# Optimization experiments

Measured on AMD Instinct MI355X. Metric: run time of the kernel, lower is better.

Reference implementation:

```python
import jax, jax.numpy as jnp
import numpy as np

L = 2048  # sequence length
V = 2048  # num_tokens == channel width (one-hot embedding)
B = 4     # batch


def _pos_bias(v_table):
    # pos[i,j] = max(i-j, 0); embed via [L,1] table -> [L,L]
    i = jnp.arange(L)
    pos = jnp.maximum(i[:, None] - i[None, :], 0)
    return v_table[pos, 0]


def setup_inputs() -> dict:
    key = jax.random.key(0)
    ks = jax.random.split(key, 11)
    idx = jax.random.randint(ks[0], (B, L), 0, V)
    lin = lambda k, std: (jax.random.normal(k, (V, V), dtype=jnp.float32) * std)
    return {
        "idx": idx,
        # layer_zero: all std=1 (explicit re-init in torch code)
        "Wq0": lin(ks[1], 1.0), "Wk0": lin(ks[2], 1.0), "Wv0": lin(ks[3], 1.0),
        # layer_one: Wk std=1 (re-init), Wv std=0.02 (default init); Wq is zero-fn
        "Wk1": lin(ks[4], 1.0), "Wv1": lin(ks[5], 0.02),
        # layer_two: Wq,Wv std=1 (re-init), Wk std=0.02 (default)
        "Wq2": lin(ks[6], 1.0), "Wk2": lin(ks[7], 0.02), "Wv2": lin(ks[8], 1.0),
        # relative-position embedding tables [L,1], std=0.02
        "v0": jax.random.normal(ks[9], (L, 1), dtype=jnp.float32) * 0.02,
        "v1": jax.random.normal(ks[10], (L, 1), dtype=jnp.float32) * 0.02,
    }


def reference(idx, Wq0, Wk0, Wv0, Wk1, Wv1, Wq2, Wk2, Wv2, v0, v1):
    e = jax.nn.one_hot(idx, V, dtype=jnp.float32)            # [B,L,V]
    tril = jnp.tril(jnp.ones((L, L), dtype=bool))
    p0 = _pos_bias(v0)                                       # [L,L]
    p1 = _pos_bias(v1)

    # layer_zero(e, e): scores = Q@K^T + sum_e(K)[:,None]*pos, tril, @V (no softmax)
    K0 = e @ Wk0.T
    Q0 = e @ Wq0.T
    V0 = e @ Wv0.T
    s0 = jnp.einsum('bqv,bkv->bqk', Q0, K0) + K0.sum(-1)[:, :, None] * p0[None]
    l0 = jnp.where(tril, s0, 0.0) @ V0                       # [B,L,V]

    # layer_one(l0, e): Wq is zero-fn -> only the pos-bias term survives
    K1 = e @ Wk1.T
    V1 = l0 @ Wv1.T
    s1 = K1.sum(-1)[:, :, None] * p1[None]
    l1 = jnp.where(tril, s1, 0.0) @ V1

    # layer_two(e, l1): v is zero-fn -> no pos bias
    K2 = l1 @ Wk2.T
    Q2 = e @ Wq2.T
    V2 = e @ Wv2.T
    s2 = jnp.einsum('bqv,bkv->bqk', Q2, K2)
    logits = jnp.where(tril, s2, 0.0) @ V2                   # [B,L,V]
    return logits
```

## Files before the change

kernel.cpp:

```cpp
#include <hip/hip_runtime.h>

typedef float f32x4 __attribute__((ext_vector_type(4)));
typedef short s16x8 __attribute__((ext_vector_type(8)));

constexpr int L = 2048;
constexpr int V = 2048;
constexpr int NB = 4;
constexpr size_t VV  = (size_t)V * V;
constexpr size_t BLV = (size_t)NB * L * V;
constexpr size_t LV  = (size_t)L * V;

__device__ __forceinline__ unsigned short f2bf(float f) {
    unsigned u = __float_as_uint(f);
    u = (u + 0x7FFFu + ((u >> 16) & 1u)) >> 16;
    return (unsigned short)u;
}
__device__ __forceinline__ float bf2f(unsigned short s) {
    return __uint_as_float(((unsigned)s) << 16);
}

__device__ __forceinline__ void gload16(const unsigned short* g, unsigned short* l) {
    auto gp = (const __attribute__((address_space(1))) unsigned int*)g;
    auto lp = (__attribute__((address_space(3))) unsigned int*)l;
    __builtin_amdgcn_global_load_lds(gp, lp, 16, 0, 0);
}

#define SBAR __builtin_amdgcn_sched_barrier(0)


__device__ __forceinline__ void stage_half(const unsigned short* G, int r0, int k0,
                                           unsigned short* slice, int wave, int lane) {
    int rl = lane >> 2, slot = lane & 3;
    #pragma unroll
    for (int r = 0; r < 2; ++r) {
        int rowl = r * 128 + wave * 16 + rl;
        int colg = k0 + ((slot ^ ((rowl >> 1) & 3)) * 8);
        gload16(G + (size_t)(r0 + rowl) * 2048 + colg,
                slice + (size_t)(r * 128 + wave * 16) * 32);
    }
}

__device__ __forceinline__ s16x8 fragx(const unsigned short* slice, int row, int kc) {
    return *(const s16x8*)&slice[row * 32 + ((kc ^ ((row >> 1) & 3)) * 8)];
}

__device__ __forceinline__ void kloop32(const unsigned short* Ab, const unsigned short* Bb,
                                        int m0, int n0, int NT, unsigned short* lds,
                                        int wave, int lane, int wr, int wc,
                                        f32x4 (&acc)[8][4]) {
    const int r15 = lane & 15, kc = lane >> 4;

    stage_half(Ab, m0, 0,  lds + 0,     wave, lane);
    stage_half(Bb, n0, 0,  lds + 8192,  wave, lane);
    stage_half(Ab, m0, 32, lds + 16384, wave, lane);
    stage_half(Bb, n0, 32, lds + 24576, wave, lane);
    asm volatile("s_waitcnt vmcnt(4)" ::: "memory");
    __builtin_amdgcn_s_barrier();
    SBAR;

    int cb = 0;
    for (int t = 0; t < NT; ++t) {
        const unsigned short* cur = lds + cb * 16384;
        int sb = cb + 2; if (sb >= 3) sb -= 3;
        unsigned short* stg = lds + sb * 16384;
        const bool pre = (t + 2 < NT);
        const int k2 = (t + 2) * 32;

        s16x8 b0[4], a[4], a2[4];
        #pragma unroll
        for (int nf = 0; nf < 4; ++nf)
            b0[nf] = fragx(cur + 8192, wc * 64 + nf * 16 + r15, kc);
        #pragma unroll
        for (int mf = 0; mf < 4; ++mf)
            a[mf] = fragx(cur, wr * 128 + mf * 16 + r15, kc);
        if (pre) stage_half(Ab, m0, k2, stg, wave, lane);
        __builtin_amdgcn_s_setprio(1);
        #pragma unroll
        for (int mf = 0; mf < 4; ++mf)
            #pragma unroll
            for (int nf = 0; nf < 4; ++nf)
                acc[mf][nf] = __builtin_amdgcn_mfma_f32_16x16x32_bf16(a[mf], b0[nf], acc[mf][nf], 0, 0, 0);
        __builtin_amdgcn_s_setprio(0);

        #pragma unroll
        for (int mf = 0; mf < 4; ++mf)
            a2[mf] = fragx(cur, wr * 128 + (mf + 4) * 16 + r15, kc);
        if (pre) stage_half(Bb, n0, k2, stg + 8192, wave, lane);
        __builtin_amdgcn_s_setprio(1);
        #pragma unroll
        for (int mf = 0; mf < 4; ++mf)
            #pragma unroll
            for (int nf = 0; nf < 4; ++nf)
                acc[mf + 4][nf] = __builtin_amdgcn_mfma_f32_16x16x32_bf16(a2[mf], b0[nf], acc[mf + 4][nf], 0, 0, 0);
        __builtin_amdgcn_s_setprio(0);

        if (pre)               { asm volatile("s_waitcnt vmcnt(4)" ::: "memory"); }
        else if (t + 2 == NT)  { asm volatile("s_waitcnt vmcnt(0)" ::: "memory"); }
        __builtin_amdgcn_s_barrier();
        SBAR;
        if (++cb == 3) cb = 0;
    }
}

template<int OUTM, bool TOEP>
__global__ __launch_bounds__(512, 2) void gemm_big(
    const unsigned short* __restrict__ A, size_t sA,
    const unsigned short* __restrict__ B, size_t sB,
    float* __restrict__ outF, unsigned short* __restrict__ outH, size_t sO,
    const int* __restrict__ idxp, const float* __restrict__ ks)
{
    __shared__ __align__(16) unsigned short lds[3 * 16384];

    const int tid  = threadIdx.x;
    const int lane = tid & 63, wave = tid >> 6;
    const int wr = wave >> 2, wc = wave & 3;
    const int bz = blockIdx.z;
    int bx = blockIdx.x, by = blockIdx.y;
    if constexpr (TOEP) { int tswap = bx; bx = by; by = tswap; }
    const int m0 = by * 256, n0 = bx * 256;
    const int r15 = lane & 15, kc = lane >> 4;

    const unsigned short* Ab = A + (size_t)bz * sA;
    const unsigned short* Bb = B + (size_t)bz * sB;
    const int NT = TOEP ? 8 * (bx + 1) : 64;

    f32x4 acc[8][4];
    const f32x4 zf = {0.f, 0.f, 0.f, 0.f};
    #pragma unroll
    for (int i = 0; i < 8; ++i)
        #pragma unroll
        for (int j = 0; j < 4; ++j) acc[i][j] = zf;

    kloop32(Ab, Bb, m0, n0, NT, lds, wave, lane, wr, wc, acc);

    float csc[4];
    if constexpr (TOEP) {
        #pragma unroll
        for (int nf = 0; nf < 4; ++nf) {
            int gcol = n0 + wc * 64 + nf * 16 + r15;
            csc[nf] = ks[idxp[bz * L + gcol]];
        }
    }
    #pragma unroll
    for (int mf = 0; mf < 8; ++mf) {
        #pragma unroll
        for (int r = 0; r < 4; ++r) {
            int grow = m0 + wr * 128 + mf * 16 + kc * 4 + r;
            #pragma unroll
            for (int nf = 0; nf < 4; ++nf) {
                float v = acc[mf][nf][r];
                if constexpr (TOEP) v *= csc[nf];
                int gcol = n0 + wc * 64 + nf * 16 + r15;
                size_t o = (size_t)bz * sO + (size_t)grow * 2048 + gcol;
                if constexpr (OUTM == 0) outF[o] = v;
                else                     outH[o] = f2bf(v);
            }
        }
    }
}

struct PDesc { const unsigned short* A; const unsigned short* B; float* oF; unsigned short* oH; };

__global__ __launch_bounds__(512, 2) void gemm_pre_big(PDesc d0, PDesc d1, PDesc d2) {
    PDesc d = (blockIdx.z == 0) ? d0 : (blockIdx.z == 1) ? d1 : d2;
    __shared__ __align__(16) unsigned short lds[3 * 16384];

    const int tid  = threadIdx.x;
    const int lane = tid & 63, wave = tid >> 6;
    const int wr = wave >> 2, wc = wave & 3;
    const int m0 = blockIdx.y * 256, n0 = blockIdx.x * 256;
    const int r15 = lane & 15, kc = lane >> 4;

    f32x4 acc[8][4];
    const f32x4 zf = {0.f, 0.f, 0.f, 0.f};
    #pragma unroll
    for (int i = 0; i < 8; ++i)
        #pragma unroll
        for (int j = 0; j < 4; ++j) acc[i][j] = zf;

    kloop32(d.A, d.B, m0, n0, 64, lds, wave, lane, wr, wc, acc);

    const bool isF = (d.oF != nullptr);
    #pragma unroll
    for (int mf = 0; mf < 8; ++mf) {
        #pragma unroll
        for (int r = 0; r < 4; ++r) {
            int grow = m0 + wr * 128 + mf * 16 + kc * 4 + r;
            #pragma unroll
            for (int nf = 0; nf < 4; ++nf) {
                float v = acc[mf][nf][r];
                int gcol = n0 + wc * 64 + nf * 16 + r15;
                size_t o = (size_t)grow * 2048 + gcol;
                if (isF) d.oF[o] = v;
                else     d.oH[o] = f2bf(v);
            }
        }
    }
}

__global__ __launch_bounds__(512, 2) void gemm_preK(const unsigned short* __restrict__ A,
                                                    const unsigned short* __restrict__ B,
                                                    float* __restrict__ outP) {
    __shared__ __align__(16) unsigned short lds[3 * 16384];

    const int tid  = threadIdx.x;
    const int lane = tid & 63, wave = tid >> 6;
    const int wr = wave >> 2, wc = wave & 3;
    const int m0 = blockIdx.y * 256, n0 = blockIdx.x * 256;
    const int r15 = lane & 15, kc = lane >> 4;
    const int z = blockIdx.z;

    const unsigned short* Ab = A + z * 512;
    const unsigned short* Bb = B + z * 512;
    float* outF = outP + (size_t)z * VV;

    f32x4 acc[8][4];
    const f32x4 zf = {0.f, 0.f, 0.f, 0.f};
    #pragma unroll
    for (int i = 0; i < 8; ++i)
        #pragma unroll
        for (int j = 0; j < 4; ++j) acc[i][j] = zf;

    kloop32(Ab, Bb, m0, n0, 16, lds, wave, lane, wr, wc, acc);

    #pragma unroll
    for (int mf = 0; mf < 8; ++mf) {
        #pragma unroll
        for (int r = 0; r < 4; ++r) {
            int grow = m0 + wr * 128 + mf * 16 + kc * 4 + r;
            #pragma unroll
            for (int nf = 0; nf < 4; ++nf) {
                int gcol = n0 + wc * 64 + nf * 16 + r15;
                outF[(size_t)grow * 2048 + gcol] = acc[mf][nf][r];
            }
        }
    }
}

__global__ __launch_bounds__(256) void reduce4_cast(const float* __restrict__ P,
                                                    unsigned short* __restrict__ H) {
    int i = blockIdx.x * 256 + threadIdx.x;
    const float4* p0 = (const float4*)P;
    const float4* p1 = (const float4*)(P + VV);
    const float4* p2 = (const float4*)(P + 2 * VV);
    const float4* p3 = (const float4*)(P + 3 * VV);
    float4 a = p0[i], b = p1[i], c = p2[i], d = p3[i];
    ushort4 h;
    h.x = f2bf(a.x + b.x + c.x + d.x);
    h.y = f2bf(a.y + b.y + c.y + d.y);
    h.z = f2bf(a.z + b.z + c.z + d.z);
    h.w = f2bf(a.w + b.w + c.w + d.w);
    ((ushort4*)H)[i] = h;
}


__global__ __launch_bounds__(256) void colsum_atomic(const float* __restrict__ W,
                                                     float* __restrict__ out) {
    int r0 = blockIdx.x * 8;
    int c = threadIdx.x;
    float s[8];
    #pragma unroll
    for (int i = 0; i < 8; ++i) s[i] = 0.f;
    for (int r = 0; r < 8; ++r) {
        const float* row = W + (size_t)(r0 + r) * V;
        #pragma unroll
        for (int i = 0; i < 8; ++i) s[i] += row[c + i * 256];
    }
    #pragma unroll
    for (int i = 0; i < 8; ++i) atomicAdd(&out[c + i * 256], s[i]);
}

__global__ void init_kernel(float* __restrict__ ks0, float* __restrict__ ks1) {
    int i = blockIdx.x * 256 + threadIdx.x;
    if (i < 2048) { ks0[i] = 0.f; ks1[i] = 0.f; }
}

__global__ __launch_bounds__(256) void tb_fill(const float* __restrict__ v1,
                                               unsigned short* __restrict__ TBh) {
    int n = blockIdx.x;
    int c0 = threadIdx.x * 8;
    s16x8 hv;
    #pragma unroll
    for (int i = 0; i < 8; ++i) {
        int k = c0 + i;
        float f = (k <= n) ? v1[n - k] : 0.f;
        hv[i] = (short)f2bf(f);
    }
    *(s16x8*)&TBh[(size_t)n * 2048 + c0] = hv;
}

struct TDesc { const float* A; unsigned short* Th; };

__global__ void transpose_cast_multi(TDesc d0, TDesc d1, TDesc d2, TDesc d3, TDesc d4) {
    TDesc d;
    switch (blockIdx.z) {
        case 0: d = d0; break;
        case 1: d = d1; break;
        case 2: d = d2; break;
        case 3: d = d3; break;
        default: d = d4; break;
    }
    __shared__ float tile[32][33];
    int x = blockIdx.x * 32 + threadIdx.x;
    int y0 = blockIdx.y * 32;
    for (int r = threadIdx.y; r < 32; r += 8)
        tile[r][threadIdx.x] = d.A[(size_t)(y0 + r) * V + x];
    __syncthreads();
    int xo = blockIdx.y * 32 + threadIdx.x;
    int yo0 = blockIdx.x * 32;
    for (int r = threadIdx.y; r < 32; r += 8)
        d.Th[(size_t)(yo0 + r) * V + xo] = f2bf(tile[threadIdx.x][r]);
}

__global__ __launch_bounds__(256) void cast_kernel(const float* __restrict__ A,
                                                   unsigned short* __restrict__ H,
                                                   int n4) {
    int i = blockIdx.x * 256 + threadIdx.x;
    if (i >= n4) return;
    float4 f = ((const float4*)A)[i];
    ushort4 h;
    h.x = f2bf(f.x); h.y = f2bf(f.y); h.z = f2bf(f.z); h.w = f2bf(f.w);
    ((ushort4*)H)[i] = h;
}


__global__ __launch_bounds__(256) void scatterA_kernel(const int* __restrict__ idx,
                                                       const float* __restrict__ G0,
                                                       const float* __restrict__ ks0,
                                                       const float* __restrict__ v0,
                                                       unsigned short* __restrict__ Th) {
    __shared__ float buck[4 * 2048];
    int tid = threadIdx.x;
    const float4 z4 = make_float4(0.f, 0.f, 0.f, 0.f);
    #pragma unroll
    for (int i = 0; i < 8; ++i) ((float4*)buck)[tid + i * 256] = z4;
    __syncthreads();

    int b = blockIdx.y, q0 = blockIdx.x * 4;
    int qr = tid >> 6, lane = tid & 63;
    int q = q0 + qr;
    const int* idxb = idx + b * L;
    int iq = idxb[q];
    float kq = ks0[iq];
    const float* Grow = G0 + (size_t)iq * V;
    float* brow = buck + qr * 2048;

    int k = lane;
    for (; k + 192 <= q; k += 256) {
        int i0 = idxb[k], i1 = idxb[k + 64], i2 = idxb[k + 128], i3 = idxb[k + 192];
        float g0 = Grow[i0], g1 = Grow[i1], g2 = Grow[i2], g3 = Grow[i3];
        float w0 = v0[q - k], w1 = v0[q - k - 64], w2 = v0[q - k - 128], w3 = v0[q - k - 192];
        atomicAdd(&brow[i0], g0 + kq * w0);
        atomicAdd(&brow[i1], g1 + kq * w1);
        atomicAdd(&brow[i2], g2 + kq * w2);
        atomicAdd(&brow[i3], g3 + kq * w3);
    }
    for (; k <= q; k += 64) {
        int ik = idxb[k];
        atomicAdd(&brow[ik], Grow[ik] + kq * v0[q - k]);
    }
    __syncthreads();
    size_t base = ((size_t)b * L + q0) * V;
    #pragma unroll
    for (int it = 0; it < 4; ++it) {
        int i = tid + it * 256;
        s16x8 hv;
        #pragma unroll
        for (int j = 0; j < 8; ++j) hv[j] = (short)f2bf(buck[i * 8 + j]);
        *(s16x8*)&Th[base + (size_t)i * 8] = hv;
    }
}

__global__ __launch_bounds__(256) void scatterC_kernel(const int* __restrict__ idx,
                                                       const unsigned short* __restrict__ T2h,
                                                       unsigned short* __restrict__ Th) {
    __shared__ float buck[4 * 2048];
    int tid = threadIdx.x;
    const float4 z4 = make_float4(0.f, 0.f, 0.f, 0.f);
    #pragma unroll
    for (int i = 0; i < 8; ++i) ((float4*)buck)[tid + i * 256] = z4;
    __syncthreads();

    int b = blockIdx.y, q0 = blockIdx.x * 4;
    int qr = tid >> 6, lane = tid & 63;
    int q = q0 + qr;
    const int* idxb = idx + b * L;
    int iq = idxb[q];
    const unsigned short* Trow = T2h + ((size_t)b * V + iq) * L;
    float* brow = buck + qr * 2048;

    int k = lane;
    for (; k + 192 <= q; k += 256) {
        int i0 = idxb[k], i1 = idxb[k + 64], i2 = idxb[k + 128], i3 = idxb[k + 192];
        float t0 = bf2f(Trow[k]), t1 = bf2f(Trow[k + 64]);
        float t2 = bf2f(Trow[k + 128]), t3 = bf2f(Trow[k + 192]);
        atomicAdd(&brow[i0], t0);
        atomicAdd(&brow[i1], t1);
        atomicAdd(&brow[i2], t2);
        atomicAdd(&brow[i3], t3);
    }
    for (; k <= q; k += 64)
        atomicAdd(&brow[idxb[k]], bf2f(Trow[k]));
    __syncthreads();
    size_t base = ((size_t)b * L + q0) * V;
    #pragma unroll
    for (int it = 0; it < 4; ++it) {
        int i = tid + it * 256;
        s16x8 hv;
        #pragma unroll
        for (int j = 0; j < 8; ++j) hv[j] = (short)f2bf(buck[i * 8 + j]);
        *(s16x8*)&Th[base + (size_t)i * 8] = hv;
    }
}


extern "C" void kernel_launch(void* const* d_in, const int* in_sizes, int n_in,
                              void* d_out, int out_size, void* d_ws, size_t ws_size,
                              hipStream_t stream) {
    (void)in_sizes; (void)n_in; (void)out_size; (void)ws_size;
    const int*   idx = (const int*)d_in[0];
    const float* Wq0 = (const float*)d_in[1];
    const float* Wk0 = (const float*)d_in[2];
    const float* Wv0 = (const float*)d_in[3];
    const float* Wk1 = (const float*)d_in[4];
    const float* Wv1 = (const float*)d_in[5];
    const float* Wq2 = (const float*)d_in[6];
    const float* Wk2 = (const float*)d_in[7];
    const float* Wv2 = (const float*)d_in[8];
    const float* v0  = (const float*)d_in[9];
    const float* v1  = (const float*)d_in[10];
    float* out = (float*)d_out;

    char* W = (char*)d_ws;
    const size_t MiB = 1024 * 1024;

    unsigned short* PPT = (unsigned short*)W;
    unsigned short* TAh = (unsigned short*)W;
    unsigned short* T2h = (unsigned short*)W;
    float* Rp = (float*)(W + 8 * MiB);
    unsigned short* Y1 = (unsigned short*)(W + 64 * MiB);
    unsigned short* Y2 = (unsigned short*)(W + 72 * MiB);
    unsigned short* Uh  = (unsigned short*)(W + 64 * MiB);
    unsigned short* TCh = Uh;
    float* Gf = (float*)(W + 96 * MiB);
    unsigned short* Y4 = (unsigned short*)(W + 112 * MiB);
    unsigned short* X1 = (unsigned short*)(W + 128 * MiB);
    unsigned short* X2 = (unsigned short*)(W + 136 * MiB);
    unsigned short* X3 = (unsigned short*)(W + 144 * MiB);
    unsigned short* X4 = (unsigned short*)(W + 152 * MiB);
    unsigned short* TBh = X3;
    float* ks0 = (float*)(W + 192 * MiB);
    float* ks1 = (float*)(W + 192 * MiB + 16 * 1024);

    dim3 blk(256);

    {
        TDesc t0{Wq0, X1}, t1{Wk0, X2}, t2{Wq2, X3}, t3{Wk2, X4}, t4{Wv0, Y1};
        transpose_cast_multi<<<dim3(64, 64, 5), dim3(32, 8), 0, stream>>>(t0, t1, t2, t3, t4);
    }
    cast_kernel<<<dim3((int)(VV / 4 / 256)), blk, 0, stream>>>(Wv1, Y2, (int)(VV / 4));
    init_kernel<<<dim3(8), blk, 0, stream>>>(ks0, ks1);
    colsum_atomic<<<dim3(256), blk, 0, stream>>>(Wk0, ks0);
    colsum_atomic<<<dim3(256), blk, 0, stream>>>(Wk1, ks1);

    {
        PDesc dG{X1, X2, Gf, nullptr};
        PDesc dM{X3, X4, nullptr, Y4};
        PDesc dP{Y1, Y2, nullptr, PPT};
        gemm_pre_big<<<dim3(8, 8, 3), dim3(512), 0, stream>>>(dG, dM, dP);
    }
    tb_fill<<<dim3(2048), blk, 0, stream>>>(v1, TBh);
    gemm_preK<<<dim3(8, 8, 4), dim3(512), 0, stream>>>(Y4, PPT, Rp);
    reduce4_cast<<<dim3((int)(VV / 4 / 256)), blk, 0, stream>>>(Rp, X1);

    scatterA_kernel<<<dim3(L / 4, NB), blk, 0, stream>>>(idx, Gf, ks0, v0, TAh);

    gemm_big<1, false><<<dim3(8, 8, NB), dim3(512), 0, stream>>>(
        X1, 0, TAh, LV, nullptr, Uh, LV, nullptr, nullptr);

    gemm_big<1, true><<<dim3(8, 8, NB), dim3(512), 0, stream>>>(
        Uh, LV, TBh, 0, nullptr, T2h, LV, idx, ks1);

    scatterC_kernel<<<dim3(L / 4, NB), blk, 0, stream>>>(idx, T2h, TCh);

    cast_kernel<<<dim3((int)(VV / 4 / 256)), blk, 0, stream>>>(Wv2, X2, (int)(VV / 4));

    gemm_big<0, false><<<dim3(8, 32, 1), dim3(512), 0, stream>>>(
        TCh, 0, X2, 0, out, nullptr, 0, nullptr, nullptr);
}
```

Measured before the change: 473.2 us.

## Split triangular Toeplitz GEMM along K, add XCD block swizzle, merge small kernels

The triangular (TOEP) GEMM now splits its K range into two halves across extra grid z-blocks. Each half writes a separate bf16 partial buffer, and scatterC sums the two partials, which evens out load imbalance from the triangular work. Non-Toeplitz GEMMs and the pre-GEMMs remap block indices with an XCD-aware swizzle to improve L2 locality per chiplet. The two cast launches and the two colsum launches are each fused into one, and the Wv2 cast is moved earlier into its own buffer. The cost is an extra partial buffer of writes and reads, plus a second bf16 rounding before the partials are summed.

```diff
diff --git a/kernel.cpp b/kernel.cpp
--- a/kernel.cpp
+++ b/kernel.cpp
@@ -45,15 +45,15 @@
 }
 
 __device__ __forceinline__ void kloop32(const unsigned short* Ab, const unsigned short* Bb,
-                                        int m0, int n0, int NT, unsigned short* lds,
+                                        int m0, int n0, int kt0, int NT, unsigned short* lds,
                                         int wave, int lane, int wr, int wc,
                                         f32x4 (&acc)[8][4]) {
     const int r15 = lane & 15, kc = lane >> 4;
 
-    stage_half(Ab, m0, 0,  lds + 0,     wave, lane);
-    stage_half(Bb, n0, 0,  lds + 8192,  wave, lane);
-    stage_half(Ab, m0, 32, lds + 16384, wave, lane);
-    stage_half(Bb, n0, 32, lds + 24576, wave, lane);
+    stage_half(Ab, m0, kt0 * 32,        lds + 0,     wave, lane);
+    stage_half(Bb, n0, kt0 * 32,        lds + 8192,  wave, lane);
+    stage_half(Ab, m0, (kt0 + 1) * 32,  lds + 16384, wave, lane);
+    stage_half(Bb, n0, (kt0 + 1) * 32,  lds + 24576, wave, lane);
     asm volatile("s_waitcnt vmcnt(4)" ::: "memory");
     __builtin_amdgcn_s_barrier();
     SBAR;
@@ -64,7 +64,7 @@
         int sb = cb + 2; if (sb >= 3) sb -= 3;
         unsigned short* stg = lds + sb * 16384;
         const bool pre = (t + 2 < NT);
-        const int k2 = (t + 2) * 32;
+        const int k2 = (kt0 + t + 2) * 32;
 
         s16x8 b0[4], a[4], a2[4];
         #pragma unroll
@@ -100,6 +100,10 @@
         SBAR;
         if (++cb == 3) cb = 0;
     }
+}
+
+__device__ __forceinline__ int xcd_swz(int flat, int total) {
+    return (flat & 7) * (total >> 3) + (flat >> 3);
 }
 
 template<int OUTM, bool TOEP>
@@ -114,15 +118,33 @@
     const int tid  = threadIdx.x;
     const int lane = tid & 63, wave = tid >> 6;
     const int wr = wave >> 2, wc = wave & 3;
-    const int bz = blockIdx.z;
-    int bx = blockIdx.x, by = blockIdx.y;
-    if constexpr (TOEP) { int tswap = bx; bx = by; by = tswap; }
+    const int r15 = lane & 15, kc = lane >> 4;
+
+    int bx, by, bz, half = 0;
+    if constexpr (TOEP) {
+        bx = blockIdx.y; by = blockIdx.x;
+        bz = blockIdx.z & 3;
+        half = blockIdx.z >> 2;
+    } else {
+        int gx = gridDim.x, gy = gridDim.y;
+        int flat = blockIdx.x + gx * (blockIdx.y + gy * blockIdx.z);
+        int total = gx * gy * gridDim.z;
+        int n2 = xcd_swz(flat, total);
+        bx = n2 % gx; n2 /= gx; by = n2 % gy; bz = n2 / gy;
+    }
     const int m0 = by * 256, n0 = bx * 256;
-    const int r15 = lane & 15, kc = lane >> 4;
+
+    int kt0 = 0, NT;
+    if constexpr (TOEP) {
+        int NTh = 4 * (bx + 1);
+        kt0 = half * NTh;
+        NT = NTh;
+    } else {
+        NT = 64;
+    }
 
     const unsigned short* Ab = A + (size_t)bz * sA;
     const unsigned short* Bb = B + (size_t)bz * sB;
-    const int NT = TOEP ? 8 * (bx + 1) : 64;
 
     f32x4 acc[8][4];
     const f32x4 zf = {0.f, 0.f, 0.f, 0.f};
@@ -131,7 +153,7 @@
         #pragma unroll
         for (int j = 0; j < 4; ++j) acc[i][j] = zf;
 
-    kloop32(Ab, Bb, m0, n0, NT, lds, wave, lane, wr, wc, acc);
+    kloop32(Ab, Bb, m0, n0, kt0, NT, lds, wave, lane, wr, wc, acc);
 
     float csc[4];
     if constexpr (TOEP) {
@@ -141,6 +163,8 @@
             csc[nf] = ks[idxp[bz * L + gcol]];
         }
     }
+    unsigned short* oH = outH;
+    if constexpr (TOEP) oH += (size_t)half * BLV;
     #pragma unroll
     for (int mf = 0; mf < 8; ++mf) {
         #pragma unroll
@@ -153,7 +177,7 @@
                 int gcol = n0 + wc * 64 + nf * 16 + r15;
                 size_t o = (size_t)bz * sO + (size_t)grow * 2048 + gcol;
                 if constexpr (OUTM == 0) outF[o] = v;
-                else                     outH[o] = f2bf(v);
+                else                     oH[o] = f2bf(v);
             }
         }
     }
@@ -162,14 +186,20 @@
 struct PDesc { const unsigned short* A; const unsigned short* B; float* oF; unsigned short* oH; };
 
 __global__ __launch_bounds__(512, 2) void gemm_pre_big(PDesc d0, PDesc d1, PDesc d2) {
-    PDesc d = (blockIdx.z == 0) ? d0 : (blockIdx.z == 1) ? d1 : d2;
     __shared__ __align__(16) unsigned short lds[3 * 16384];
 
     const int tid  = threadIdx.x;
     const int lane = tid & 63, wave = tid >> 6;
     const int wr = wave >> 2, wc = wave & 3;
-    const int m0 = blockIdx.y * 256, n0 = blockIdx.x * 256;
     const int r15 = lane & 15, kc = lane >> 4;
+
+    int flat = blockIdx.x + 8 * (blockIdx.y + 8 * blockIdx.z);
+    int total = 64 * gridDim.z;
+    int n2 = xcd_swz(flat, total);
+    int bx = n2 & 7; n2 >>= 3;
+    int by = n2 & 7; n2 >>= 3;
+    PDesc d = (n2 == 0) ? d0 : (n2 == 1) ? d1 : d2;
+    const int m0 = by * 256, n0 = bx * 256;
 
     f32x4 acc[8][4];
     const f32x4 zf = {0.f, 0.f, 0.f, 0.f};
@@ -178,7 +208,7 @@
         #pragma unroll
         for (int j = 0; j < 4; ++j) acc[i][j] = zf;
 
-    kloop32(d.A, d.B, m0, n0, 64, lds, wave, lane, wr, wc, acc);
+    kloop32(d.A, d.B, m0, n0, 0, 64, lds, wave, lane, wr, wc, acc);
 
     const bool isF = (d.oF != nullptr);
     #pragma unroll
@@ -206,9 +236,14 @@
     const int tid  = threadIdx.x;
     const int lane = tid & 63, wave = tid >> 6;
     const int wr = wave >> 2, wc = wave & 3;
-    const int m0 = blockIdx.y * 256, n0 = blockIdx.x * 256;
     const int r15 = lane & 15, kc = lane >> 4;
-    const int z = blockIdx.z;
+
+    int flat = blockIdx.x + 8 * (blockIdx.y + 8 * blockIdx.z);
+    int n2 = xcd_swz(flat, 256);
+    int bx = n2 & 7; n2 >>= 3;
+    int by = n2 & 7; n2 >>= 3;
+    int z = n2;
+    const int m0 = by * 256, n0 = bx * 256;
 
     const unsigned short* Ab = A + z * 512;
     const unsigned short* Bb = B + z * 512;
@@ -221,7 +256,7 @@
         #pragma unroll
         for (int j = 0; j < 4; ++j) acc[i][j] = zf;
 
-    kloop32(Ab, Bb, m0, n0, 16, lds, wave, lane, wr, wc, acc);
+    kloop32(Ab, Bb, m0, n0, 0, 16, lds, wave, lane, wr, wc, acc);
 
     #pragma unroll
     for (int mf = 0; mf < 8; ++mf) {
@@ -254,8 +289,10 @@
 }
 
 
-__global__ __launch_bounds__(256) void colsum_atomic(const float* __restrict__ W,
-                                                     float* __restrict__ out) {
+__global__ __launch_bounds__(256) void colsum2(const float* __restrict__ W0, float* __restrict__ o0,
+                                               const float* __restrict__ W1, float* __restrict__ o1) {
+    const float* W = blockIdx.y ? W1 : W0;
+    float* out = blockIdx.y ? o1 : o0;
     int r0 = blockIdx.x * 8;
     int c = threadIdx.x;
     float s[8];
@@ -312,11 +349,13 @@
         d.Th[(size_t)(yo0 + r) * V + xo] = f2bf(tile[threadIdx.x][r]);
 }
 
-__global__ __launch_bounds__(256) void cast_kernel(const float* __restrict__ A,
-                                                   unsigned short* __restrict__ H,
-                                                   int n4) {
+__global__ __launch_bounds__(256) void cast2_kernel(const float* __restrict__ A0,
+                                                    unsigned short* __restrict__ H0,
+                                                    const float* __restrict__ A1,
+                                                    unsigned short* __restrict__ H1) {
+    const float* A = blockIdx.y ? A1 : A0;
+    unsigned short* H = blockIdx.y ? H1 : H0;
     int i = blockIdx.x * 256 + threadIdx.x;
-    if (i >= n4) return;
     float4 f = ((const float4*)A)[i];
     ushort4 h;
     h.x = f2bf(f.x); h.y = f2bf(f.y); h.z = f2bf(f.z); h.w = f2bf(f.w);
@@ -372,7 +411,8 @@
 }
 
 __global__ __launch_bounds__(256) void scatterC_kernel(const int* __restrict__ idx,
-                                                       const unsigned short* __restrict__ T2h,
+                                                       const unsigned short* __restrict__ T2a,
+                                                       const unsigned short* __restrict__ T2b,
                                                        unsigned short* __restrict__ Th) {
     __shared__ float buck[4 * 2048];
     int tid = threadIdx.x;
@@ -386,21 +426,25 @@
     int q = q0 + qr;
     const int* idxb = idx + b * L;
     int iq = idxb[q];
-    const unsigned short* Trow = T2h + ((size_t)b * V + iq) * L;
+    size_t roff = ((size_t)b * V + iq) * L;
+    const unsigned short* TrA = T2a + roff;
+    const unsigned short* TrB = T2b + roff;
     float* brow = buck + qr * 2048;
 
     int k = lane;
     for (; k + 192 <= q; k += 256) {
         int i0 = idxb[k], i1 = idxb[k + 64], i2 = idxb[k + 128], i3 = idxb[k + 192];
-        float t0 = bf2f(Trow[k]), t1 = bf2f(Trow[k + 64]);
-        float t2 = bf2f(Trow[k + 128]), t3 = bf2f(Trow[k + 192]);
+        float t0 = bf2f(TrA[k]) + bf2f(TrB[k]);
+        float t1 = bf2f(TrA[k + 64]) + bf2f(TrB[k + 64]);
+        float t2 = bf2f(TrA[k + 128]) + bf2f(TrB[k + 128]);
+        float t3 = bf2f(TrA[k + 192]) + bf2f(TrB[k + 192]);
         atomicAdd(&brow[i0], t0);
         atomicAdd(&brow[i1], t1);
         atomicAdd(&brow[i2], t2);
         atomicAdd(&brow[i3], t3);
     }
     for (; k <= q; k += 64)
-        atomicAdd(&brow[idxb[k]], bf2f(Trow[k]));
+        atomicAdd(&brow[idxb[k]], bf2f(TrA[k]) + bf2f(TrB[k]));
     __syncthreads();
     size_t base = ((size_t)b * L + q0) * V;
     #pragma unroll
@@ -436,7 +480,8 @@
 
     unsigned short* PPT = (unsigned short*)W;
     unsigned short* TAh = (unsigned short*)W;
-    unsigned short* T2h = (unsigned short*)W;
+    unsigned short* T2a = (unsigned short*)W;
+    unsigned short* T2b = T2a + BLV;
     float* Rp = (float*)(W + 8 * MiB);
     unsigned short* Y1 = (unsigned short*)(W + 64 * MiB);
     unsigned short* Y2 = (unsigned short*)(W + 72 * MiB);
@@ -448,7 +493,8 @@
     unsigned short* X2 = (unsigned short*)(W + 136 * MiB);
     unsigned short* X3 = (unsigned short*)(W + 144 * MiB);
     unsigned short* X4 = (unsigned short*)(W + 152 * MiB);
-    unsigned short* TBh = X3;
+    unsigned short* X5 = (unsigned short*)(W + 160 * MiB);
+    unsigned short* TBh = (unsigned short*)(W + 168 * MiB);
     float* ks0 = (float*)(W + 192 * MiB);
     float* ks1 = (float*)(W + 192 * MiB + 16 * 1024);
 
@@ -458,10 +504,10 @@
         TDesc t0{Wq0, X1}, t1{Wk0, X2}, t2{Wq2, X3}, t3{Wk2, X4}, t4{Wv0, Y1};
         transpose_cast_multi<<<dim3(64, 64, 5), dim3(32, 8), 0, stream>>>(t0, t1, t2, t3, t4);
     }
-    cast_kernel<<<dim3((int)(VV / 4 / 256)), blk, 0, stream>>>(Wv1, Y2, (int)(VV / 4));
+    cast2_kernel<<<dim3((int)(VV / 4 / 256), 2), blk, 0, stream>>>(Wv1, Y2, Wv2, X5);
+    tb_fill<<<dim3(2048), blk, 0, stream>>>(v1, TBh);
     init_kernel<<<dim3(8), blk, 0, stream>>>(ks0, ks1);
-    colsum_atomic<<<dim3(256), blk, 0, stream>>>(Wk0, ks0);
-    colsum_atomic<<<dim3(256), blk, 0, stream>>>(Wk1, ks1);
+    colsum2<<<dim3(256, 2), blk, 0, stream>>>(Wk0, ks0, Wk1, ks1);
 
     {
         PDesc dG{X1, X2, Gf, nullptr};
@@ -469,7 +515,6 @@
         PDesc dP{Y1, Y2, nullptr, PPT};
         gemm_pre_big<<<dim3(8, 8, 3), dim3(512), 0, stream>>>(dG, dM, dP);
     }
-    tb_fill<<<dim3(2048), blk, 0, stream>>>(v1, TBh);
     gemm_preK<<<dim3(8, 8, 4), dim3(512), 0, stream>>>(Y4, PPT, Rp);
     reduce4_cast<<<dim3((int)(VV / 4 / 256)), blk, 0, stream>>>(Rp, X1);
 
@@ -478,13 +523,11 @@
     gemm_big<1, false><<<dim3(8, 8, NB), dim3(512), 0, stream>>>(
         X1, 0, TAh, LV, nullptr, Uh, LV, nullptr, nullptr);
 
-    gemm_big<1, true><<<dim3(8, 8, NB), dim3(512), 0, stream>>>(
-        Uh, LV, TBh, 0, nullptr, T2h, LV, idx, ks1);
-
-    scatterC_kernel<<<dim3(L / 4, NB), blk, 0, stream>>>(idx, T2h, TCh);
-
-    cast_kernel<<<dim3((int)(VV / 4 / 256)), blk, 0, stream>>>(Wv2, X2, (int)(VV / 4));
+    gemm_big<1, true><<<dim3(8, 8, 2 * NB), dim3(512), 0, stream>>>(
+        Uh, LV, TBh, 0, nullptr, T2a, LV, idx, ks1);
+
+    scatterC_kernel<<<dim3(L / 4, NB), blk, 0, stream>>>(idx, T2a, T2b, TCh);
 
     gemm_big<0, false><<<dim3(8, 32, 1), dim3(512), 0, stream>>>(
-        TCh, 0, X2, 0, out, nullptr, 0, nullptr, nullptr);
-}
+        TCh, 0, X5, 0, out, nullptr, 0, nullptr, nullptr);
+}
```

Measured after the change: 463.6 us. 2.0% less time.
